# Kernel tuning notes

Measured on AMD Instinct MI355X. Metric: run time of the kernel, lower is better.

## Reference

```python
import jax, jax.numpy as jnp
import numpy as np

N = 1048576
NUM_LEVELS = 16; LEVEL_DIM = 2; BASE_RES = 16; TABLE = 1 << 19
BOUND = 1.0; DESIRED = 64
_s = np.exp(np.log(DESIRED / BASE_RES) / (NUM_LEVELS - 1))
RESOLUTIONS = [int(np.floor(BASE_RES * _s ** l)) for l in range(NUM_LEVELS)]
OFFS = np.array([[(i >> 0) & 1, (i >> 1) & 1, (i >> 2) & 1] for i in range(8)], dtype=np.int32)
PRIMES = (1, 2654435761, 805459861)


def _corner_index(corner, R):
    # corner: [N,8,3] int32 in [0,R]. Dense index if grid fits in table, else spatial hash.
    if (R + 1) ** 3 <= TABLE:
        stride = jnp.array([1, R + 1, (R + 1) ** 2], dtype=jnp.int32)
        return jnp.sum(corner * stride, axis=-1)
    c = corner.astype(jnp.uint32)
    h = (c[..., 0] * jnp.uint32(PRIMES[0])) ^ (c[..., 1] * jnp.uint32(PRIMES[1])) ^ (c[..., 2] * jnp.uint32(PRIMES[2]))
    return (h % jnp.uint32(TABLE)).astype(jnp.int32)


def hashgrid_encode(x, embeddings):
    # x: [N,3] in [-BOUND,BOUND]; embeddings: [L, TABLE, C]
    pos = (x + BOUND) / (2.0 * BOUND)  # [0,1]
    offs = jnp.asarray(OFFS)  # [8,3]
    outs = []
    for l, R in enumerate(RESOLUTIONS):  # fixed small loop over levels
        xg = pos * R
        x0 = jnp.clip(jnp.floor(xg).astype(jnp.int32), 0, R - 1)  # [N,3]
        f = xg - x0.astype(xg.dtype)  # trilinear fractions [N,3]
        corners = x0[:, None, :] + offs[None]  # [N,8,3]
        idx = _corner_index(corners, R)  # [N,8]
        feats = embeddings[l][idx]  # [N,8,C] irregular gather
        w = jnp.prod(jnp.where(offs[None] == 1, f[:, None, :], 1.0 - f[:, None, :]), axis=-1)  # [N,8]
        outs.append(jnp.sum(feats * w[..., None], axis=1))  # [N,C]
    return jnp.concatenate(outs, axis=-1)  # [N, L*C] = [N,32]


def sh_encode(d):
    # degree-4 real spherical harmonics (16 coeffs), torch-ngp convention
    x, y, z = d[..., 0], d[..., 1], d[..., 2]
    xx, yy, zz = x * x, y * y, z * z
    xy, yz, xz = x * y, y * z, x * z
    return jnp.stack([
        0.28209479177387814 * jnp.ones_like(x),
        -0.48860251190291987 * y,
        0.48860251190291987 * z,
        -0.48860251190291987 * x,
        1.0925484305920792 * xy,
        -1.0925484305920792 * yz,
        0.94617469575755997 * zz - 0.31539156525252005,
        -1.0925484305920792 * xz,
        0.54627421529603959 * (xx - yy),
        0.59004358992664352 * y * (yy - 3.0 * xx),
        2.8906114426405538 * xy * z,
        0.45704579946446572 * y * (1.0 - 5.0 * zz),
        0.3731763325901154 * z * (5.0 * zz - 3.0),
        0.45704579946446572 * x * (1.0 - 5.0 * zz),
        1.4453057213202769 * z * (xx - yy),
        0.59004358992664352 * x * (3.0 * yy - xx),
    ], axis=-1)  # [N,16]


def setup_inputs() -> dict:
    key = jax.random.key(0)
    ks = jax.random.split(key, 8)
    x = jax.random.uniform(ks[0], (N, 3), jnp.float32) * 2.0 - 1.0  # in [-bound, bound]
    d_raw = jax.random.normal(ks[1], (N, 3), jnp.float32)
    d = d_raw / (jnp.linalg.norm(d_raw, axis=-1, keepdims=True) + 1e-8)  # unit view dirs
    embeddings = jax.random.normal(ks[2], (NUM_LEVELS, TABLE, LEVEL_DIM), jnp.float32) * 1e-2
    def w(k, i, o):
        return jax.random.normal(k, (i, o), jnp.float32) / np.sqrt(i).astype(np.float32)
    ws0 = w(ks[3], 32, 64)
    ws1 = w(ks[4], 64, 16)
    wc0 = w(ks[5], 31, 64)
    wc1 = w(ks[6], 64, 64)
    wc2 = w(ks[7], 64, 1)
    return {"x": x, "d": d, "embeddings": embeddings,
            "ws0": ws0, "ws1": ws1, "wc0": wc0, "wc1": wc1, "wc2": wc2}


def reference(x, d, embeddings, ws0, ws1, wc0, wc1, wc2):
    # sigma branch: hashgrid encode -> 2-layer bias-free MLP
    h = hashgrid_encode(x, embeddings)          # [N,32]
    h = jax.nn.relu(h @ ws0) @ ws1              # [N,16]
    sigma = jnp.abs(h[:, :1])                   # [N,1]
    geo_feat = h[:, 1:]                         # [N,15]
    # color branch: SH encode dir, concat geo feature, 3-layer bias-free MLP
    hd = jnp.concatenate([sh_encode(d), geo_feat], axis=-1)  # [N,31]
    c = jax.nn.relu(hd @ wc0)
    c = jax.nn.relu(c @ wc1)
    color = jnp.abs(c @ wc2)                    # [N,1]
    return sigma, color
```

## Files before the change

### kernel.cpp

```cpp
#include <hip/hip_runtime.h>
#include <cmath>

#define NPTS 1048576
#define TABLE_SZ 524288
#define NBUCK 32768

typedef _Float16 half8 __attribute__((ext_vector_type(8)));
typedef _Float16 half4 __attribute__((ext_vector_type(4)));
typedef _Float16 h2 __attribute__((ext_vector_type(2)));
typedef __fp16 fp16x2 __attribute__((ext_vector_type(2)));
typedef float floatx4 __attribute__((ext_vector_type(4)));
typedef unsigned int uint2a4 __attribute__((ext_vector_type(2), aligned(4)));

#define MFMA16x16x32 __builtin_amdgcn_mfma_f32_16x16x32_f16

__device__ __forceinline__ h2 as_h2(unsigned int u) {
    union { unsigned int u; h2 h; } c; c.u = u; return c.h;
}
__device__ __forceinline__ unsigned int pk_u32(float a, float b) {
    union { fp16x2 h; unsigned int u; } c;
    c.h = __builtin_amdgcn_cvt_pkrtz(a, b);
    return c.u;
}

__global__ void prepack_weights(const float* __restrict__ ws0,
                                const float* __restrict__ ws1,
                                const float* __restrict__ wc0,
                                const float* __restrict__ wc1,
                                const float* __restrict__ wc2,
                                half8* __restrict__ wfrag)
{
    const int f = blockIdx.x, l = threadIdx.x;
    const int lane_m = l & 15, k0 = (l >> 4) * 8;
    half8 hv;

    if (f >= 6 && f < 10) {
        const int m = 16*(f-6) + lane_m;
        #pragma unroll
        for (int e = 0; e < 8; ++e) {
            const int k = k0 + e;
            float v;
            if (k < 16)       v = wc0[k*64 + m];
            else if (k == 16) v = 0.0f;
            else              v = wc0[(k-1)*64 + m];
            hv[e] = (_Float16)v;
        }
        wfrag[f*64 + l] = hv;
        return;
    }

    const float* W; int Kreal, Mreal, mt, kt;
    if (f < 4)       { W = ws0; Kreal = 32; Mreal = 64; mt = f;          kt = 0;        }
    else if (f < 6)  { W = ws1; Kreal = 64; Mreal = 16; mt = 0;          kt = f - 4;    }
    else if (f < 18) { W = wc1; Kreal = 64; Mreal = 64; mt = (f-10)>>1;  kt = (f-10)&1; }
    else             { W = wc2; Kreal = 64; Mreal = 1;  mt = 0;          kt = f - 18;   }

    const int m  = 16*mt + lane_m;
    const int kk0 = 32*kt + k0;
    #pragma unroll
    for (int e = 0; e < 8; ++e) {
        const int k = kk0 + e;
        const float v = (m < Mreal && k < Kreal) ? W[k*Mreal + m] : 0.0f;
        hv[e] = (_Float16)v;
    }
    wfrag[f*64 + l] = hv;
}

__global__ __launch_bounds__(256) void convert_tables(
    const float* __restrict__ emb, unsigned int* __restrict__ tabu,
    unsigned int* __restrict__ hist, int zero_hist,
    int4 ra, int4 rb, int4 rc, int4 rd,
    int4 oa, int4 ob, int4 oc, int4 od)
{
    const int l = blockIdx.y;
    if (l == 16) {
        if (zero_hist) {
            const int e = blockIdx.x * 256 + threadIdx.x;
            if (e < NBUCK) hist[e] = 0u;
        }
        return;
    }
    const int q = l >> 2, j = l & 3;
    const int4 rv = (q == 0) ? ra : (q == 1) ? rb : (q == 2) ? rc : rd;
    const int4 ov = (q == 0) ? oa : (q == 1) ? ob : (q == 2) ? oc : od;
    const int R   = (j == 0) ? rv.x : (j == 1) ? rv.y : (j == 2) ? rv.z : rv.w;
    const int off = (j == 0) ? ov.x : (j == 1) ? ov.y : (j == 2) ? ov.z : ov.w;
    const int n = (R+1)*(R+1)*(R+1);
    const int e = blockIdx.x * 256 + threadIdx.x;
    if (e >= n) return;
    const float2 v = *(const float2*)(emb + (size_t)l * (TABLE_SZ*2) + 2*(size_t)e);
    tabu[off + e] = pk_u32(v.x, v.y);
}

__device__ __forceinline__ int bucket_of(float px, float py, float pz) {
    int bx = (int)(px * 32.0f); bx = bx < 0 ? 0 : (bx > 31 ? 31 : bx);
    int by = (int)(py * 32.0f); by = by < 0 ? 0 : (by > 31 ? 31 : by);
    int bz = (int)(pz * 32.0f); bz = bz < 0 ? 0 : (bz > 31 ? 31 : bz);
    return bx | (by << 5) | (bz << 10);
}

__global__ __launch_bounds__(256) void hist_kernel(
    const float* __restrict__ xin, unsigned int* __restrict__ hist,
    unsigned int* __restrict__ rnk)
{
    const int i = blockIdx.x * 256 + threadIdx.x;
    const float px = (xin[3*i+0] + 1.0f) * 0.5f;
    const float py = (xin[3*i+1] + 1.0f) * 0.5f;
    const float pz = (xin[3*i+2] + 1.0f) * 0.5f;
    rnk[i] = atomicAdd(&hist[bucket_of(px, py, pz)], 1u);
}

__global__ __launch_bounds__(1024) void scan_kernel(
    const unsigned int* __restrict__ hist, unsigned int* __restrict__ off)
{
    __shared__ unsigned int ssum[1024];
    const int t = threadIdx.x;
    unsigned int v[32];
    unsigned int s = 0;
    #pragma unroll
    for (int j = 0; j < 32; ++j) {
        const unsigned int h = hist[t*32 + j];
        v[j] = s; s += h;
    }
    ssum[t] = s;
    __syncthreads();
    for (int d = 1; d < 1024; d <<= 1) {
        const unsigned int add = (t >= d) ? ssum[t-d] : 0u;
        __syncthreads();
        ssum[t] += add;
        __syncthreads();
    }
    const unsigned int base = (t == 0) ? 0u : ssum[t-1];
    #pragma unroll
    for (int j = 0; j < 32; ++j) off[t*32 + j] = base + v[j];
}

__global__ __launch_bounds__(256) void scatter_kernel(
    const float* __restrict__ xin, const unsigned int* __restrict__ boff,
    const unsigned int* __restrict__ rnk, float4* __restrict__ xs4)
{
    const int i = blockIdx.x * 256 + threadIdx.x;
    const float px = (xin[3*i+0] + 1.0f) * 0.5f;
    const float py = (xin[3*i+1] + 1.0f) * 0.5f;
    const float pz = (xin[3*i+2] + 1.0f) * 0.5f;
    const int b = bucket_of(px, py, pz);
    const unsigned int pos = boff[b] + rnk[i];
    xs4[pos] = make_float4(px, py, pz, __uint_as_float((unsigned int)i));
}

__global__ __launch_bounds__(256, 4) void ngp_gather_sorted(
    const float4* __restrict__ xs4, const unsigned int* __restrict__ tabu,
    _Float16* __restrict__ feats,
    int4 ra, int4 rb, int4 rc, int4 rd,
    int4 oa, int4 ob, int4 oc, int4 od)
{
    const int p = blockIdx.x * 256 + threadIdx.x;
    const int q = blockIdx.y;

    const float4 xv = xs4[p];
    const float px = xv.x, py = xv.y, pz = xv.z;

    const int4 rv = (q == 0) ? ra : (q == 1) ? rb : (q == 2) ? rc : rd;
    const int4 ov = (q == 0) ? oa : (q == 1) ? ob : (q == 2) ? oc : od;

    uint2a4 P[16];
    float fx[4], fy[4], fz[4];

    #pragma unroll
    for (int j = 0; j < 4; ++j) {
        const int R   = (j == 0) ? rv.x : (j == 1) ? rv.y : (j == 2) ? rv.z : rv.w;
        const int off = (j == 0) ? ov.x : (j == 1) ? ov.y : (j == 2) ? ov.z : ov.w;
        const float Rf = (float)R;
        const float gx = px*Rf, gy = py*Rf, gz = pz*Rf;
        int x0 = (int)floorf(gx); x0 = x0 < 0 ? 0 : (x0 > R-1 ? R-1 : x0);
        int y0 = (int)floorf(gy); y0 = y0 < 0 ? 0 : (y0 > R-1 ? R-1 : y0);
        int z0 = (int)floorf(gz); z0 = z0 < 0 ? 0 : (z0 > R-1 ? R-1 : z0);
        fx[j] = gx - (float)x0; fy[j] = gy - (float)y0; fz[j] = gz - (float)z0;
        const int s1 = R + 1, s2 = s1 * s1;
        const unsigned int* tab = tabu + off;
        const int b = x0 + y0*s1 + z0*s2;
        P[4*j+0] = *(const uint2a4*)(tab + b);
        P[4*j+1] = *(const uint2a4*)(tab + b + s1);
        P[4*j+2] = *(const uint2a4*)(tab + b + s2);
        P[4*j+3] = *(const uint2a4*)(tab + b + s1 + s2);
    }

    union { half8 v; h2 h[4]; } hv;
    #pragma unroll
    for (int j = 0; j < 4; ++j) {
        const _Float16 fxh = (_Float16)fx[j];
        const _Float16 fyh = (_Float16)fy[j];
        const _Float16 fzh = (_Float16)fz[j];
        const h2 fx2 = {fxh, fxh}, fy2 = {fyh, fyh}, fz2 = {fzh, fzh};
        const h2 c000 = as_h2(P[4*j+0].x), c100 = as_h2(P[4*j+0].y);
        const h2 c010 = as_h2(P[4*j+1].x), c110 = as_h2(P[4*j+1].y);
        const h2 c001 = as_h2(P[4*j+2].x), c101 = as_h2(P[4*j+2].y);
        const h2 c011 = as_h2(P[4*j+3].x), c111 = as_h2(P[4*j+3].y);
        const h2 a00 = c000 + fx2 * (c100 - c000);
        const h2 a10 = c010 + fx2 * (c110 - c010);
        const h2 a01 = c001 + fx2 * (c101 - c001);
        const h2 a11 = c011 + fx2 * (c111 - c011);
        const h2 b0  = a00 + fy2 * (a10 - a00);
        const h2 b1  = a01 + fy2 * (a11 - a01);
        hv.h[j] = b0 + fz2 * (b1 - b0);
    }
    *(half8*)&feats[((size_t)q * NPTS + p) * 8] = hv.v;
}

__global__ __launch_bounds__(256, 4) void ngp_gather_lin(
    const float* __restrict__ xin, const unsigned int* __restrict__ tabu,
    _Float16* __restrict__ feats,
    int4 ra, int4 rb, int4 rc, int4 rd,
    int4 oa, int4 ob, int4 oc, int4 od)
{
    const int tid = blockIdx.x * 256 + threadIdx.x;
    const int p = tid >> 2;
    const int q = tid & 3;

    const float px = (xin[3*p+0] + 1.0f) * 0.5f;
    const float py = (xin[3*p+1] + 1.0f) * 0.5f;
    const float pz = (xin[3*p+2] + 1.0f) * 0.5f;

    const int4 rv = (q == 0) ? ra : (q == 1) ? rb : (q == 2) ? rc : rd;
    const int4 ov = (q == 0) ? oa : (q == 1) ? ob : (q == 2) ? oc : od;

    uint2a4 P[16];
    float fx[4], fy[4], fz[4];
    #pragma unroll
    for (int j = 0; j < 4; ++j) {
        const int R   = (j == 0) ? rv.x : (j == 1) ? rv.y : (j == 2) ? rv.z : rv.w;
        const int off = (j == 0) ? ov.x : (j == 1) ? ov.y : (j == 2) ? ov.z : ov.w;
        const float Rf = (float)R;
        const float gx = px*Rf, gy = py*Rf, gz = pz*Rf;
        int x0 = (int)floorf(gx); x0 = x0 < 0 ? 0 : (x0 > R-1 ? R-1 : x0);
        int y0 = (int)floorf(gy); y0 = y0 < 0 ? 0 : (y0 > R-1 ? R-1 : y0);
        int z0 = (int)floorf(gz); z0 = z0 < 0 ? 0 : (z0 > R-1 ? R-1 : z0);
        fx[j] = gx - (float)x0; fy[j] = gy - (float)y0; fz[j] = gz - (float)z0;
        const int s1 = R + 1, s2 = s1 * s1;
        const unsigned int* tab = tabu + off;
        const int b = x0 + y0*s1 + z0*s2;
        P[4*j+0] = *(const uint2a4*)(tab + b);
        P[4*j+1] = *(const uint2a4*)(tab + b + s1);
        P[4*j+2] = *(const uint2a4*)(tab + b + s2);
        P[4*j+3] = *(const uint2a4*)(tab + b + s1 + s2);
    }
    union { half8 v; h2 h[4]; } hv;
    #pragma unroll
    for (int j = 0; j < 4; ++j) {
        const _Float16 fxh = (_Float16)fx[j];
        const _Float16 fyh = (_Float16)fy[j];
        const _Float16 fzh = (_Float16)fz[j];
        const h2 fx2 = {fxh, fxh}, fy2 = {fyh, fyh}, fz2 = {fzh, fzh};
        const h2 c000 = as_h2(P[4*j+0].x), c100 = as_h2(P[4*j+0].y);
        const h2 c010 = as_h2(P[4*j+1].x), c110 = as_h2(P[4*j+1].y);
        const h2 c001 = as_h2(P[4*j+2].x), c101 = as_h2(P[4*j+2].y);
        const h2 c011 = as_h2(P[4*j+3].x), c111 = as_h2(P[4*j+3].y);
        const h2 a00 = c000 + fx2 * (c100 - c000);
        const h2 a10 = c010 + fx2 * (c110 - c010);
        const h2 a01 = c001 + fx2 * (c101 - c001);
        const h2 a11 = c011 + fx2 * (c111 - c011);
        const h2 b0  = a00 + fy2 * (a10 - a00);
        const h2 b1  = a01 + fy2 * (a11 - a01);
        hv.h[j] = b0 + fz2 * (b1 - b0);
    }
    *(half8*)&feats[(size_t)p*32 + q*8] = hv.v;
}

template<int SORTED>
__global__ __launch_bounds__(256) void ngp_mlp(
    const float* __restrict__ din, const _Float16* __restrict__ feats,
    const float4* __restrict__ xs4,
    const half8* __restrict__ wfrag, float* __restrict__ out)
{
    __shared__ __align__(16) _Float16 smM[4][32][88];

    const int tid  = threadIdx.x;
    const int w    = tid >> 6, lane = tid & 63;
    const int gbase = (blockIdx.x * 4 + w) * 32;

    const int n = lane & 15, g = lane >> 4;
    const floatx4 zz = {0.f, 0.f, 0.f, 0.f};

    unsigned int orig0, orig1;
    if (SORTED) {
        orig0 = __float_as_uint(xs4[gbase + n].w);
        orig1 = __float_as_uint(xs4[gbase + 16 + n].w);
    } else {
        orig0 = gbase + n;
        orig1 = gbase + 16 + n;
    }

    const float dX0 = din[3*orig0+0], dY0 = din[3*orig0+1], dZ0 = din[3*orig0+2];
    const float dX1 = din[3*orig1+0], dY1 = din[3*orig1+1], dZ1 = din[3*orig1+2];

    auto storeQ = [&](int pt, int mt, floatx4 a) {
        union { unsigned int u[2]; half4 v; } c;
        c.u[0] = pk_u32(fmaxf(a[0], 0.f), fmaxf(a[1], 0.f));
        c.u[1] = pk_u32(fmaxf(a[2], 0.f), fmaxf(a[3], 0.f));
        *(half4*)&smM[w][pt][16*mt + 4*g] = c.v;
    };

    {
        const half8 A0 = wfrag[0*64+lane], A1 = wfrag[1*64+lane];
        const half8 A2 = wfrag[2*64+lane], A3 = wfrag[3*64+lane];
        half8 B0, B1;
        if (SORTED) {
            B0 = *(const half8*)&feats[((size_t)g * NPTS + (gbase + n)) * 8];
            B1 = *(const half8*)&feats[((size_t)g * NPTS + (gbase + 16 + n)) * 8];
        } else {
            B0 = *(const half8*)&feats[(size_t)(gbase + n)*32 + 8*g];
            B1 = *(const half8*)&feats[(size_t)(gbase + 16 + n)*32 + 8*g];
        }
        #pragma unroll
        for (int nt = 0; nt < 2; ++nt) {
            const int pt = nt*16 + n;
            const half8 B = nt ? B1 : B0;
            floatx4 a0 = MFMA16x16x32(A0, B, zz, 0,0,0);
            floatx4 a1 = MFMA16x16x32(A1, B, zz, 0,0,0);
            floatx4 a2 = MFMA16x16x32(A2, B, zz, 0,0,0);
            floatx4 a3 = MFMA16x16x32(A3, B, zz, 0,0,0);
            storeQ(pt, 0, a0); storeQ(pt, 1, a1); storeQ(pt, 2, a2); storeQ(pt, 3, a3);
        }
    }
    asm volatile("" ::: "memory");

    unsigned int s1w0_0, s1w0_1, s1w1_0, s1w1_1;
    {
        const half8 A0 = wfrag[4*64+lane], A1 = wfrag[5*64+lane];
        float sig0, sig1;
        {
            const int pt = n;
            const half8 B0 = *(const half8*)&smM[w][pt][ 0 + 8*g];
            const half8 B1 = *(const half8*)&smM[w][pt][32 + 8*g];
            floatx4 acc = MFMA16x16x32(A0, B0, zz, 0,0,0);
            acc = MFMA16x16x32(A1, B1, acc, 0,0,0);
            s1w0_0 = pk_u32(acc[0], acc[1]);
            s1w0_1 = pk_u32(acc[2], acc[3]);
            sig0 = acc[0];
        }
        {
            const int pt = 16 + n;
            const half8 B0 = *(const half8*)&smM[w][pt][ 0 + 8*g];
            const half8 B1 = *(const half8*)&smM[w][pt][32 + 8*g];
            floatx4 acc = MFMA16x16x32(A0, B0, zz, 0,0,0);
            acc = MFMA16x16x32(A1, B1, acc, 0,0,0);
            s1w1_0 = pk_u32(acc[0], acc[1]);
            s1w1_1 = pk_u32(acc[2], acc[3]);
            sig1 = acc[0];
        }
        if (g == 0) {
            out[orig0] = fabsf(sig0);
            out[orig1] = fabsf(sig1);
        }
    }
    asm volatile("" ::: "memory");

    {
        const half8 A0 = wfrag[6*64+lane], A1 = wfrag[7*64+lane];
        const half8 A2 = wfrag[8*64+lane], A3 = wfrag[9*64+lane];
        const int srcA = ((g & 1) << 5) + n;
        #pragma unroll
        for (int nt = 0; nt < 2; ++nt) {
            const int pt = nt*16 + n;
            const unsigned int v0 = nt ? s1w1_0 : s1w0_0;
            const unsigned int v1 = nt ? s1w1_1 : s1w0_1;
            const unsigned int w0 = __shfl(v0, srcA);
            const unsigned int w1 = __shfl(v1, srcA);
            const unsigned int w2 = __shfl(v0, srcA + 16);
            const unsigned int w3 = __shfl(v1, srcA + 16);
            union { half8 v; unsigned int u[4]; } B;
            if (g < 2) {
                const float x = nt ? dX1 : dX0;
                const float y = nt ? dY1 : dY0;
                const float z = nt ? dZ1 : dZ0;
                const float xx = x*x, yy = y*y, zzq = z*z;
                const float xy = x*y, yz = y*z, xz = x*z;
                float s[8];
                if (g == 0) {
                    s[0] = 0.28209479177387814f;
                    s[1] = -0.48860251190291987f * y;
                    s[2] =  0.48860251190291987f * z;
                    s[3] = -0.48860251190291987f * x;
                    s[4] =  1.0925484305920792f * xy;
                    s[5] = -1.0925484305920792f * yz;
                    s[6] =  0.94617469575756f * zzq - 0.31539156525252005f;
                    s[7] = -1.0925484305920792f * xz;
                } else {
                    s[0] =  0.5462742152960396f * (xx - yy);
                    s[1] =  0.5900435899266435f * y * (yy - 3.0f*xx);
                    s[2] =  2.890611442640554f * xy * z;
                    s[3] =  0.4570457994644657f * y * (1.0f - 5.0f*zzq);
                    s[4] =  0.3731763325901154f * z * (5.0f*zzq - 3.0f);
                    s[5] =  0.4570457994644657f * x * (1.0f - 5.0f*zzq);
                    s[6] =  1.445305721320277f * z * (xx - yy);
                    s[7] =  0.5900435899266435f * x * (3.0f*yy - xx);
                }
                B.u[0] = pk_u32(s[0], s[1]); B.u[1] = pk_u32(s[2], s[3]);
                B.u[2] = pk_u32(s[4], s[5]); B.u[3] = pk_u32(s[6], s[7]);
            } else {
                B.u[0] = w0; B.u[1] = w1; B.u[2] = w2; B.u[3] = w3;
            }
            floatx4 a0 = MFMA16x16x32(A0, B.v, zz, 0,0,0);
            floatx4 a1 = MFMA16x16x32(A1, B.v, zz, 0,0,0);
            floatx4 a2 = MFMA16x16x32(A2, B.v, zz, 0,0,0);
            floatx4 a3 = MFMA16x16x32(A3, B.v, zz, 0,0,0);
            storeQ(pt, 0, a0); storeQ(pt, 1, a1); storeQ(pt, 2, a2); storeQ(pt, 3, a3);
        }
    }
    asm volatile("" ::: "memory");

    {
        const half8 A0 = wfrag[10*64+lane], A1 = wfrag[11*64+lane];
        const half8 A2 = wfrag[12*64+lane], A3 = wfrag[13*64+lane];
        const half8 A4 = wfrag[14*64+lane], A5 = wfrag[15*64+lane];
        const half8 A6 = wfrag[16*64+lane], A7 = wfrag[17*64+lane];
        #pragma unroll
        for (int nt = 0; nt < 2; ++nt) {
            const int pt = nt*16 + n;
            const half8 B0 = *(const half8*)&smM[w][pt][ 0 + 8*g];
            const half8 B1 = *(const half8*)&smM[w][pt][32 + 8*g];
            floatx4 a0 = MFMA16x16x32(A0, B0, zz, 0,0,0); a0 = MFMA16x16x32(A1, B1, a0, 0,0,0);
            floatx4 a1 = MFMA16x16x32(A2, B0, zz, 0,0,0); a1 = MFMA16x16x32(A3, B1, a1, 0,0,0);
            floatx4 a2 = MFMA16x16x32(A4, B0, zz, 0,0,0); a2 = MFMA16x16x32(A5, B1, a2, 0,0,0);
            floatx4 a3 = MFMA16x16x32(A6, B0, zz, 0,0,0); a3 = MFMA16x16x32(A7, B1, a3, 0,0,0);
            storeQ(pt, 0, a0); storeQ(pt, 1, a1); storeQ(pt, 2, a2); storeQ(pt, 3, a3);
        }
    }
    asm volatile("" ::: "memory");

    {
        const half8 A0 = wfrag[18*64+lane], A1 = wfrag[19*64+lane];
        #pragma unroll
        for (int nt = 0; nt < 2; ++nt) {
            const int pt = nt*16 + n;
            const half8 B0 = *(const half8*)&smM[w][pt][ 0 + 8*g];
            const half8 B1 = *(const half8*)&smM[w][pt][32 + 8*g];
            floatx4 acc = MFMA16x16x32(A0, B0, zz, 0,0,0);
            acc = MFMA16x16x32(A1, B1, acc, 0,0,0);
            if (g == 0) out[NPTS + (nt ? orig1 : orig0)] = fabsf(acc[0]);
        }
    }
}

extern "C" void kernel_launch(void* const* d_in, const int* in_sizes, int n_in,
                              void* d_out, int out_size, void* d_ws, size_t ws_size,
                              hipStream_t stream)
{
    const float* x   = (const float*)d_in[0];
    const float* d   = (const float*)d_in[1];
    const float* emb = (const float*)d_in[2];
    const float* ws0 = (const float*)d_in[3];
    const float* ws1 = (const float*)d_in[4];
    const float* wc0 = (const float*)d_in[5];
    const float* wc1 = (const float*)d_in[6];
    const float* wc2 = (const float*)d_in[7];
    float* out = (float*)d_out;

    const size_t OFF_WFRAG = 0;
    const size_t OFF_TABU  = 32768;
    const size_t OFF_FEATS = OFF_TABU + 8388608;
    const size_t OFF_HIST  = OFF_FEATS + 67108864;
    const size_t OFF_OFF   = OFF_HIST + NBUCK*4;
    const size_t OFF_XS4   = OFF_OFF + NBUCK*4;
    const size_t OFF_RNK   = OFF_XS4 + (size_t)NPTS*16;
    const size_t NEED_SORT = OFF_RNK + (size_t)NPTS*4;
    const size_t NEED_LIN  = OFF_HIST;

    half8* wfrag        = (half8*)((char*)d_ws + OFF_WFRAG);
    unsigned int* tabu  = (unsigned int*)((char*)d_ws + OFF_TABU);
    _Float16* feats     = (_Float16*)((char*)d_ws + OFF_FEATS);
    unsigned int* hist  = (unsigned int*)((char*)d_ws + OFF_HIST);
    unsigned int* boff  = (unsigned int*)((char*)d_ws + OFF_OFF);
    float4* xs4         = (float4*)((char*)d_ws + OFF_XS4);
    unsigned int* rnk   = (unsigned int*)((char*)d_ws + OFF_RNK);

    int r[16], off[16];
    const double s = std::exp(std::log(4.0) / 15.0);
    int acc = 0;
    for (int l = 0; l < 16; ++l) {
        r[l] = (int)std::floor(16.0 * std::pow(s, (double)l));
        off[l] = acc;
        acc += (r[l]+1)*(r[l]+1)*(r[l]+1);
    }
    const int4 ra = {r[0],  r[1],  r[2],  r[3]};
    const int4 rb = {r[4],  r[5],  r[6],  r[7]};
    const int4 rc = {r[8],  r[9],  r[10], r[11]};
    const int4 rd = {r[12], r[13], r[14], r[15]};
    const int4 oa = {off[0],  off[1],  off[2],  off[3]};
    const int4 ob = {off[4],  off[5],  off[6],  off[7]};
    const int4 oc = {off[8],  off[9],  off[10], off[11]};
    const int4 od = {off[12], off[13], off[14], off[15]};

    prepack_weights<<<20, 64, 0, stream>>>(ws0, ws1, wc0, wc1, wc2, wfrag);

    const int nmax = (r[15]+1)*(r[15]+1)*(r[15]+1);
    dim3 cgrid((nmax + 255) / 256, 17);

    if (ws_size >= NEED_SORT) {
        convert_tables<<<cgrid, 256, 0, stream>>>(emb, tabu, hist, 1, ra, rb, rc, rd, oa, ob, oc, od);
        hist_kernel<<<NPTS/256, 256, 0, stream>>>(x, hist, rnk);
        scan_kernel<<<1, 1024, 0, stream>>>(hist, boff);
        scatter_kernel<<<NPTS/256, 256, 0, stream>>>(x, boff, rnk, xs4);
        dim3 ggrid(NPTS/256, 4);
        ngp_gather_sorted<<<ggrid, 256, 0, stream>>>(xs4, tabu, feats, ra, rb, rc, rd, oa, ob, oc, od);
        ngp_mlp<1><<<NPTS/128, 256, 0, stream>>>(d, feats, xs4, wfrag, out);
    } else if (ws_size >= NEED_LIN) {
        convert_tables<<<cgrid, 256, 0, stream>>>(emb, tabu, hist, 0, ra, rb, rc, rd, oa, ob, oc, od);
        ngp_gather_lin<<<NPTS*4/256, 256, 0, stream>>>(x, tabu, feats, ra, rb, rc, rd, oa, ob, oc, od);
        ngp_mlp<0><<<NPTS/128, 256, 0, stream>>>(d, feats, (const float4*)nullptr, wfrag, out);
    }
}
```

Before: 194.1 us.

## Scatter view directions into sorted order and process 64 points per MLP wave

The scatter kernel now also writes view directions permuted into bucket-sorted order (with the original index), so the MLP reads them contiguously instead of gathering din through a permutation. Each MLP wavefront now handles 64 points instead of 32, halving the grid, reusing the weight fragments across more points and reshaping the shared buffer to 64x72. The cost is an extra 16 MB workspace buffer plus its write traffic, and higher register and LDS use per wave.

```diff
diff --git a/kernel.cpp b/kernel.cpp
--- a/kernel.cpp
+++ b/kernel.cpp
@@ -136,8 +136,9 @@
 }
 
 __global__ __launch_bounds__(256) void scatter_kernel(
-    const float* __restrict__ xin, const unsigned int* __restrict__ boff,
-    const unsigned int* __restrict__ rnk, float4* __restrict__ xs4)
+    const float* __restrict__ xin, const float* __restrict__ din,
+    const unsigned int* __restrict__ boff, const unsigned int* __restrict__ rnk,
+    float4* __restrict__ xs4, float4* __restrict__ ds4)
 {
     const int i = blockIdx.x * 256 + threadIdx.x;
     const float px = (xin[3*i+0] + 1.0f) * 0.5f;
@@ -146,6 +147,10 @@
     const int b = bucket_of(px, py, pz);
     const unsigned int pos = boff[b] + rnk[i];
     xs4[pos] = make_float4(px, py, pz, __uint_as_float((unsigned int)i));
+    if (ds4) {
+        const float dx = din[3*i+0], dy = din[3*i+1], dz = din[3*i+2];
+        ds4[pos] = make_float4(dx, dy, dz, __uint_as_float((unsigned int)i));
+    }
 }
 
 __global__ __launch_bounds__(256, 4) void ngp_gather_sorted(
@@ -266,32 +271,38 @@
     *(half8*)&feats[(size_t)p*32 + q*8] = hv.v;
 }
 
-template<int SORTED>
+template<int MODE>
 __global__ __launch_bounds__(256) void ngp_mlp(
     const float* __restrict__ din, const _Float16* __restrict__ feats,
-    const float4* __restrict__ xs4,
+    const float4* __restrict__ xs4, const float4* __restrict__ ds4,
     const half8* __restrict__ wfrag, float* __restrict__ out)
 {
-    __shared__ __align__(16) _Float16 smM[4][32][88];
+    __shared__ __align__(16) _Float16 smM[4][64][72];
 
     const int tid  = threadIdx.x;
     const int w    = tid >> 6, lane = tid & 63;
-    const int gbase = (blockIdx.x * 4 + w) * 32;
+    const int gbase = (blockIdx.x * 4 + w) * 64;
 
     const int n = lane & 15, g = lane >> 4;
     const floatx4 zz = {0.f, 0.f, 0.f, 0.f};
 
-    unsigned int orig0, orig1;
-    if (SORTED) {
-        orig0 = __float_as_uint(xs4[gbase + n].w);
-        orig1 = __float_as_uint(xs4[gbase + 16 + n].w);
-    } else {
-        orig0 = gbase + n;
-        orig1 = gbase + 16 + n;
-    }
-
-    const float dX0 = din[3*orig0+0], dY0 = din[3*orig0+1], dZ0 = din[3*orig0+2];
-    const float dX1 = din[3*orig1+0], dY1 = din[3*orig1+1], dZ1 = din[3*orig1+2];
+    unsigned int orig[4];
+    float dX[4], dY[4], dZ[4];
+    #pragma unroll
+    for (int nt = 0; nt < 4; ++nt) {
+        const int pt = nt*16 + n;
+        if (MODE == 2) {
+            const float4 dv = ds4[gbase + pt];
+            dX[nt] = dv.x; dY[nt] = dv.y; dZ[nt] = dv.z;
+            orig[nt] = __float_as_uint(dv.w);
+        } else if (MODE == 1) {
+            orig[nt] = __float_as_uint(xs4[gbase + pt].w);
+            dX[nt] = din[3*orig[nt]+0]; dY[nt] = din[3*orig[nt]+1]; dZ[nt] = din[3*orig[nt]+2];
+        } else {
+            orig[nt] = gbase + pt;
+            dX[nt] = din[3*orig[nt]+0]; dY[nt] = din[3*orig[nt]+1]; dZ[nt] = din[3*orig[nt]+2];
+        }
+    }
 
     auto storeQ = [&](int pt, int mt, floatx4 a) {
         union { unsigned int u[2]; half4 v; } c;
@@ -303,18 +314,14 @@
     {
         const half8 A0 = wfrag[0*64+lane], A1 = wfrag[1*64+lane];
         const half8 A2 = wfrag[2*64+lane], A3 = wfrag[3*64+lane];
-        half8 B0, B1;
-        if (SORTED) {
-            B0 = *(const half8*)&feats[((size_t)g * NPTS + (gbase + n)) * 8];
-            B1 = *(const half8*)&feats[((size_t)g * NPTS + (gbase + 16 + n)) * 8];
-        } else {
-            B0 = *(const half8*)&feats[(size_t)(gbase + n)*32 + 8*g];
-            B1 = *(const half8*)&feats[(size_t)(gbase + 16 + n)*32 + 8*g];
-        }
         #pragma unroll
-        for (int nt = 0; nt < 2; ++nt) {
+        for (int nt = 0; nt < 4; ++nt) {
             const int pt = nt*16 + n;
-            const half8 B = nt ? B1 : B0;
+            half8 B;
+            if (MODE >= 1)
+                B = *(const half8*)&feats[((size_t)g * NPTS + (gbase + pt)) * 8];
+            else
+                B = *(const half8*)&feats[(size_t)(gbase + pt)*32 + 8*g];
             floatx4 a0 = MFMA16x16x32(A0, B, zz, 0,0,0);
             floatx4 a1 = MFMA16x16x32(A1, B, zz, 0,0,0);
             floatx4 a2 = MFMA16x16x32(A2, B, zz, 0,0,0);
@@ -324,33 +331,19 @@
     }
     asm volatile("" ::: "memory");
 
-    unsigned int s1w0_0, s1w0_1, s1w1_0, s1w1_1;
+    unsigned int s1a[4], s1b[4];
     {
         const half8 A0 = wfrag[4*64+lane], A1 = wfrag[5*64+lane];
-        float sig0, sig1;
-        {
-            const int pt = n;
+        #pragma unroll
+        for (int nt = 0; nt < 4; ++nt) {
+            const int pt = nt*16 + n;
             const half8 B0 = *(const half8*)&smM[w][pt][ 0 + 8*g];
             const half8 B1 = *(const half8*)&smM[w][pt][32 + 8*g];
             floatx4 acc = MFMA16x16x32(A0, B0, zz, 0,0,0);
             acc = MFMA16x16x32(A1, B1, acc, 0,0,0);
-            s1w0_0 = pk_u32(acc[0], acc[1]);
-            s1w0_1 = pk_u32(acc[2], acc[3]);
-            sig0 = acc[0];
-        }
-        {
-            const int pt = 16 + n;
-            const half8 B0 = *(const half8*)&smM[w][pt][ 0 + 8*g];
-            const half8 B1 = *(const half8*)&smM[w][pt][32 + 8*g];
-            floatx4 acc = MFMA16x16x32(A0, B0, zz, 0,0,0);
-            acc = MFMA16x16x32(A1, B1, acc, 0,0,0);
-            s1w1_0 = pk_u32(acc[0], acc[1]);
-            s1w1_1 = pk_u32(acc[2], acc[3]);
-            sig1 = acc[0];
-        }
-        if (g == 0) {
-            out[orig0] = fabsf(sig0);
-            out[orig1] = fabsf(sig1);
+            s1a[nt] = pk_u32(acc[0], acc[1]);
+            s1b[nt] = pk_u32(acc[2], acc[3]);
+            if (g == 0) out[orig[nt]] = fabsf(acc[0]);
         }
     }
     asm volatile("" ::: "memory");
@@ -360,19 +353,15 @@
         const half8 A2 = wfrag[8*64+lane], A3 = wfrag[9*64+lane];
         const int srcA = ((g & 1) << 5) + n;
         #pragma unroll
-        for (int nt = 0; nt < 2; ++nt) {
+        for (int nt = 0; nt < 4; ++nt) {
             const int pt = nt*16 + n;
-            const unsigned int v0 = nt ? s1w1_0 : s1w0_0;
-            const unsigned int v1 = nt ? s1w1_1 : s1w0_1;
-            const unsigned int w0 = __shfl(v0, srcA);
-            const unsigned int w1 = __shfl(v1, srcA);
-            const unsigned int w2 = __shfl(v0, srcA + 16);
-            const unsigned int w3 = __shfl(v1, srcA + 16);
+            const unsigned int w0 = __shfl(s1a[nt], srcA);
+            const unsigned int w1 = __shfl(s1b[nt], srcA);
+            const unsigned int w2 = __shfl(s1a[nt], srcA + 16);
+            const unsigned int w3 = __shfl(s1b[nt], srcA + 16);
             union { half8 v; unsigned int u[4]; } B;
             if (g < 2) {
-                const float x = nt ? dX1 : dX0;
-                const float y = nt ? dY1 : dY0;
-                const float z = nt ? dZ1 : dZ0;
+                const float x = dX[nt], y = dY[nt], z = dZ[nt];
                 const float xx = x*x, yy = y*y, zzq = z*z;
                 const float xy = x*y, yz = y*z, xz = x*z;
                 float s[8];
@@ -415,7 +404,7 @@
         const half8 A4 = wfrag[14*64+lane], A5 = wfrag[15*64+lane];
         const half8 A6 = wfrag[16*64+lane], A7 = wfrag[17*64+lane];
         #pragma unroll
-        for (int nt = 0; nt < 2; ++nt) {
+        for (int nt = 0; nt < 4; ++nt) {
             const int pt = nt*16 + n;
             const half8 B0 = *(const half8*)&smM[w][pt][ 0 + 8*g];
             const half8 B1 = *(const half8*)&smM[w][pt][32 + 8*g];
@@ -431,13 +420,13 @@
     {
         const half8 A0 = wfrag[18*64+lane], A1 = wfrag[19*64+lane];
         #pragma unroll
-        for (int nt = 0; nt < 2; ++nt) {
+        for (int nt = 0; nt < 4; ++nt) {
             const int pt = nt*16 + n;
             const half8 B0 = *(const half8*)&smM[w][pt][ 0 + 8*g];
             const half8 B1 = *(const half8*)&smM[w][pt][32 + 8*g];
             floatx4 acc = MFMA16x16x32(A0, B0, zz, 0,0,0);
             acc = MFMA16x16x32(A1, B1, acc, 0,0,0);
-            if (g == 0) out[NPTS + (nt ? orig1 : orig0)] = fabsf(acc[0]);
+            if (g == 0) out[NPTS + orig[nt]] = fabsf(acc[0]);
         }
     }
 }
@@ -463,7 +452,9 @@
     const size_t OFF_OFF   = OFF_HIST + NBUCK*4;
     const size_t OFF_XS4   = OFF_OFF + NBUCK*4;
     const size_t OFF_RNK   = OFF_XS4 + (size_t)NPTS*16;
-    const size_t NEED_SORT = OFF_RNK + (size_t)NPTS*4;
+    const size_t OFF_DS4   = OFF_RNK + (size_t)NPTS*4;
+    const size_t NEED_SORT = OFF_DS4;
+    const size_t NEED_DS4  = OFF_DS4 + (size_t)NPTS*16;
     const size_t NEED_LIN  = OFF_HIST;
 
     half8* wfrag        = (half8*)((char*)d_ws + OFF_WFRAG);
@@ -473,6 +464,7 @@
     unsigned int* boff  = (unsigned int*)((char*)d_ws + OFF_OFF);
     float4* xs4         = (float4*)((char*)d_ws + OFF_XS4);
     unsigned int* rnk   = (unsigned int*)((char*)d_ws + OFF_RNK);
+    float4* ds4         = (float4*)((char*)d_ws + OFF_DS4);
 
     int r[16], off[16];
     const double s = std::exp(std::log(4.0) / 15.0);
@@ -497,16 +489,20 @@
     dim3 cgrid((nmax + 255) / 256, 17);
 
     if (ws_size >= NEED_SORT) {
+        const bool full = (ws_size >= NEED_DS4);
         convert_tables<<<cgrid, 256, 0, stream>>>(emb, tabu, hist, 1, ra, rb, rc, rd, oa, ob, oc, od);
         hist_kernel<<<NPTS/256, 256, 0, stream>>>(x, hist, rnk);
         scan_kernel<<<1, 1024, 0, stream>>>(hist, boff);
-        scatter_kernel<<<NPTS/256, 256, 0, stream>>>(x, boff, rnk, xs4);
+        scatter_kernel<<<NPTS/256, 256, 0, stream>>>(x, d, boff, rnk, xs4, full ? ds4 : nullptr);
         dim3 ggrid(NPTS/256, 4);
         ngp_gather_sorted<<<ggrid, 256, 0, stream>>>(xs4, tabu, feats, ra, rb, rc, rd, oa, ob, oc, od);
-        ngp_mlp<1><<<NPTS/128, 256, 0, stream>>>(d, feats, xs4, wfrag, out);
+        if (full)
+            ngp_mlp<2><<<NPTS/256, 256, 0, stream>>>(d, feats, xs4, ds4, wfrag, out);
+        else
+            ngp_mlp<1><<<NPTS/256, 256, 0, stream>>>(d, feats, xs4, nullptr, wfrag, out);
     } else if (ws_size >= NEED_LIN) {
         convert_tables<<<cgrid, 256, 0, stream>>>(emb, tabu, hist, 0, ra, rb, rc, rd, oa, ob, oc, od);
         ngp_gather_lin<<<NPTS*4/256, 256, 0, stream>>>(x, tabu, feats, ra, rb, rc, rd, oa, ob, oc, od);
-        ngp_mlp<0><<<NPTS/128, 256, 0, stream>>>(d, feats, (const float4*)nullptr, wfrag, out);
-    }
-}
+        ngp_mlp<0><<<NPTS/256, 256, 0, stream>>>(d, feats, nullptr, nullptr, wfrag, out);
+    }
+}
```

Measured after the change: 190.7 us. About the same (-1.8%).
